# Kernel tuning notes

Hardware: AMD Instinct MI355X
Metric: run time of the kernel (lower is better)

## Reference

```python
import jax, jax.numpy as jnp
import numpy as np

B, L, D, H = 2, 2048, 1024, 16
DK = D // H


def setup_inputs() -> dict:
    key = jax.random.key(0)
    ks = jax.random.split(key, 12)
    s = 1.0 / np.sqrt(D)
    inp = {
        "query": jax.random.normal(ks[0], (B, L, D), jnp.float32),
        "key_": jax.random.normal(ks[1], (B, L, D), jnp.float32),
        "value": jax.random.normal(ks[2], (B, L, D), jnp.float32),
        # causal boolean mask, broadcast over heads: (B, 1, L_q, L_k)
        "mask": jnp.broadcast_to(jnp.tril(jnp.ones((L, L), jnp.bool_)), (B, 1, L, L)),
        "w_q": jax.random.uniform(ks[3], (D, D), jnp.float32, -s, s),
        "b_q": jax.random.uniform(ks[4], (D,), jnp.float32, -s, s),
        "w_k": jax.random.uniform(ks[5], (D, D), jnp.float32, -s, s),
        "b_k": jax.random.uniform(ks[6], (D,), jnp.float32, -s, s),
        "w_v": jax.random.uniform(ks[7], (D, D), jnp.float32, -s, s),
        "b_v": jax.random.uniform(ks[8], (D,), jnp.float32, -s, s),
        "w_o": jax.random.uniform(ks[9], (D, D), jnp.float32, -s, s),
        "b_o": jax.random.uniform(ks[10], (D,), jnp.float32, -s, s),
    }
    return inp


def reference(query, key_, value, mask, w_q, b_q, w_k, b_k, w_v, b_v, w_o, b_o):
    # torch nn.Linear: y = x @ W.T + b, weight shape (out, in)
    Q = query @ w_q.T + b_q
    K = key_ @ w_k.T + b_k
    V = value @ w_v.T + b_v
    # (B, L, H, DK) -> (B, H, L, DK)
    Q = Q.reshape(B, L, H, DK).transpose(0, 2, 1, 3)
    K = K.reshape(B, L, H, DK).transpose(0, 2, 1, 3)
    V = V.reshape(B, L, H, DK).transpose(0, 2, 1, 3)
    scaling = jnp.sqrt(jnp.float32(DK))
    scores = jnp.einsum("bhqd,bhkd->bhqk", Q, K) / scaling  # (B,H,L,L)
    scores = jnp.where(mask, scores, jnp.float32(-1e9))
    attn = jax.nn.softmax(scores, axis=-1)
    out = jnp.einsum("bhqk,bhkd->bhqd", attn, V)  # (B,H,L,DK)
    out = out.transpose(0, 2, 1, 3).reshape(B, L, D)
    return out @ w_o.T + b_o
```

## Files before the change

### kernel.cpp

```cpp
#include <hip/hip_runtime.h>
#include <stdint.h>

#define Bb 2
#define Ll 2048
#define Dd 1024
#define Hh 16
#define DKd 64
#define Mm (Bb*Ll)

typedef __bf16 bf16_t;
typedef __bf16 bf16x8 __attribute__((ext_vector_type(8)));
typedef float f32x4 __attribute__((ext_vector_type(4)));
typedef unsigned u32x2 __attribute__((ext_vector_type(2)));

#define AS1C(p) ((const __attribute__((address_space(1))) void*)(p))
#define AS3(p)  ((__attribute__((address_space(3))) void*)(p))

__device__ __forceinline__ unsigned short bfu(float f){
  return __builtin_bit_cast(unsigned short, (bf16_t)f);
}
__device__ __forceinline__ void wait_vm4(){ asm volatile("s_waitcnt vmcnt(4)" ::: "memory"); }
__device__ __forceinline__ void wait_vm6(){ asm volatile("s_waitcnt vmcnt(6)" ::: "memory"); }
__device__ __forceinline__ void wait_vm0(){ asm volatile("s_waitcnt vmcnt(0)" ::: "memory"); }
__device__ __forceinline__ void bar(){
  __builtin_amdgcn_sched_barrier(0);
  __builtin_amdgcn_s_barrier();
  __builtin_amdgcn_sched_barrier(0);
}

struct Cvt7 { const float* in[7]; ushort4* out[7]; int n4[7]; };

__global__ void cvt_multi(Cvt7 a){
  const int z = blockIdx.y;
  int i = blockIdx.x*256 + threadIdx.x;
  if (i < a.n4[z]){
    float4 v = ((const float4*)a.in[z])[i];
    ushort4 o; o.x=bfu(v.x); o.y=bfu(v.y); o.z=bfu(v.z); o.w=bfu(v.w);
    a.out[z][i] = o;
  }
}

#define BM 128
#define BN 64
#define BKs 64

struct GemmArgs {
  const bf16_t* A[3];
  const bf16_t* W[3];
  const float*  bias[3];
  void*         out[3];
  float         scale[3];
  int           mode[3];
};

__device__ __forceinline__ void stage_tile(
    const bf16_t* __restrict__ A, const bf16_t* __restrict__ Bw,
    int m0, int n0, int K, int k0, bf16_t* As, bf16_t* Bs,
    int w, int srow, int scol)
{
#pragma unroll
  for (int i = 0; i < 4; i++) {
    int c = i*4 + w;
    int row = c*8 + srow;
    int sc = scol ^ ((row & 7) << 3);
    __builtin_amdgcn_global_load_lds(AS1C(A + (size_t)(m0+row)*K + k0 + sc),
                                     AS3(As + c*512), 16, 0, 0);
  }
#pragma unroll
  for (int i = 0; i < 2; i++) {
    int c = i*4 + w;
    int row = c*8 + srow;
    int sc = scol ^ ((row & 7) << 3);
    __builtin_amdgcn_global_load_lds(AS1C(Bw + (size_t)(n0+row)*K + k0 + sc),
                                     AS3(Bs + c*512), 16, 0, 0);
  }
}

__global__ __launch_bounds__(256) void gemm_bt(GemmArgs ga, int M, int N, int K)
{
  const int z = blockIdx.z;
  const bf16_t* __restrict__ A  = ga.A[z];
  const bf16_t* __restrict__ Bw = ga.W[z];
  const float*  __restrict__ bias = ga.bias[z];
  void* __restrict__ out = ga.out[z];
  const float scale = ga.scale[z];
  const int mode = ga.mode[z];

  __shared__ bf16_t As[2][BM*BKs];
  __shared__ bf16_t Bs[2][BN*BKs];
  const int tid = threadIdx.x;
  const int lane = tid & 63;
  const int w = tid >> 6;
  const int m0 = blockIdx.x * BM;
  const int n0 = blockIdx.y * BN;
  const int wr = (w >> 1) * 64, wc = (w & 1) * 32;
  const int lrow16 = lane & 15;
  const int kgrp = lane >> 4;
  const int srow = lane >> 3;
  const int scol = (lane & 7) * 8;

  f32x4 acc[4][2] = {};

  stage_tile(A, Bw, m0, n0, K, 0, As[0], Bs[0], w, srow, scol);

  const int KT = K / BKs;
  int cur = 0;
  for (int kt = 0; kt < KT; ++kt) {
    if (kt + 1 < KT) {
      stage_tile(A, Bw, m0, n0, K, (kt+1)*BKs, As[cur^1], Bs[cur^1], w, srow, scol);
      wait_vm6();
    } else {
      wait_vm0();
    }
    bar();
#pragma unroll
    for (int ks = 0; ks < 2; ++ks) {
      const int kbyte = ks*64 + kgrp*16;
      bf16x8 af[4], bfr[2];
#pragma unroll
      for (int m = 0; m < 4; m++) {
        int row = wr + m*16 + lrow16;
        af[m] = *(const bf16x8*)((const char*)As[cur] + row*128 + (kbyte ^ ((row & 7) << 4)));
      }
#pragma unroll
      for (int n = 0; n < 2; n++) {
        int row = wc + n*16 + lrow16;
        bfr[n] = *(const bf16x8*)((const char*)Bs[cur] + row*128 + (kbyte ^ ((row & 7) << 4)));
      }
#pragma unroll
      for (int m = 0; m < 4; m++)
#pragma unroll
        for (int n = 0; n < 2; n++)
          acc[m][n] = __builtin_amdgcn_mfma_f32_16x16x32_bf16(af[m], bfr[n], acc[m][n], 0, 0, 0);
    }
    bar();
    cur ^= 1;
  }

#pragma unroll
  for (int m = 0; m < 4; m++)
#pragma unroll
    for (int n = 0; n < 2; n++) {
      const int row0 = m0 + wr + m*16 + kgrp*4;
      const int col  = n0 + wc + n*16 + lrow16;
      const float bcol = bias[col];
      if (mode == 2) {
        int b = row0 >> 11, l0 = row0 & 2047;
        int h = col >> 6, dk = col & 63;
        ushort4 u;
        u.x = bfu((acc[m][n][0] + bcol) * scale);
        u.y = bfu((acc[m][n][1] + bcol) * scale);
        u.z = bfu((acc[m][n][2] + bcol) * scale);
        u.w = bfu((acc[m][n][3] + bcol) * scale);
        *(ushort4*)((unsigned short*)out + ((size_t)((b<<4) + h)*DKd + dk)*Ll + l0) = u;
      } else {
#pragma unroll
        for (int i = 0; i < 4; i++) {
          int row = row0 + i;
          float v = (acc[m][n][i] + bcol) * scale;
          if (mode == 1) {
            ((float*)out)[(size_t)row*N + col] = v;
          } else {
            int b = row >> 11, l = row & 2047;
            int h = col >> 6, dk = col & 63;
            ((unsigned short*)out)[((size_t)((b<<4) + h)*Ll + l)*DKd + dk] = bfu(v);
          }
        }
      }
    }
}

#define KVB 64

__global__ __launch_bounds__(256) void attn_kernel(
    const bf16_t* __restrict__ Qh, const bf16_t* __restrict__ Kh,
    const bf16_t* __restrict__ VTg, unsigned short* __restrict__ Oa)
{
  const int id = blockIdx.x;
  const int x = id & 7;
  const int rest = id >> 3;
  const int hq = rest >> 4;
  const int j  = rest & 15;
  const int bh = x + 8*hq;
  const int sA = j;
  const int qtB = 31 - j;

  const int tid = threadIdx.x, lane = tid & 63, w = tid >> 6;
  const int r = lane & 15, g = lane >> 4;

  const bf16_t* Qp  = Qh  + (size_t)bh * Ll * DKd;
  const bf16_t* Kp  = Kh  + (size_t)bh * Ll * DKd;
  const bf16_t* VTp = VTg + (size_t)bh * Ll * DKd;

  __shared__ bf16_t Klds[2][64*64];
  __shared__ bf16_t Vlds[2][64*64];
  __shared__ bf16_t Plds[4][16*64];

  int q0 = j * 64;
  bf16x8 qf[2], qB[2];
#pragma unroll
  for (int ks = 0; ks < 2; ++ks) {
    qf[ks] = *(const bf16x8*)(Qp + (size_t)(q0 + w*16 + r)*DKd + ks*32 + g*8);
    qB[ks] = *(const bf16x8*)(Qp + (size_t)(qtB*64 + w*16 + r)*DKd + ks*32 + g*8);
  }

  bf16x8 ones;
#pragma unroll
  for (int jj = 0; jj < 8; ++jj) ones[jj] = (bf16_t)1.0f;

  f32x4 accO[4] = {};
  f32x4 accL = {};
  float mrow = -1e30f;

  const int krow_l = lane >> 3;
  const int kcol_l = ((lane & 7)*16) ^ (krow_l << 4);
  char* Pw = (char*)&Plds[w][0];
  const int rsw = (r & 7) << 4;
  const int b_ = bh >> 4, h_ = bh & 15;

  auto pre_tiles = [&](int kv, int buf){
#pragma unroll
    for (int i = 0; i < 2; ++i) {
      int c = i*4 + w;
      __builtin_amdgcn_global_load_lds(
        AS1C((const char*)Kp + (size_t)(kv*KVB + c*8 + krow_l)*128 + kcol_l),
        AS3((char*)&Klds[buf][0] + c*1024), 16, 0, 0);
      __builtin_amdgcn_global_load_lds(
        AS1C((const char*)VTp + (size_t)(c*8 + krow_l)*4096 + kv*128 + kcol_l),
        AS3((char*)&Vlds[buf][0] + c*1024), 16, 0, 0);
    }
  };

  pre_tiles(0, 0);

  int cur = 0;
  for (int s = 0; s < 33; ++s) {
    if (s < 32) {
      int kv2 = (s < sA) ? s + 1 : s - sA;
      pre_tiles(kv2, cur^1);
      wait_vm4();
    } else {
      wait_vm0();
    }
    bar();

    const int kv0 = ((s <= sA) ? s : s - sA - 1) * KVB;

    const char* Kbase = (const char*)&Klds[cur][0];
    f32x4 sv[4] = {};
    __builtin_amdgcn_s_setprio(1);
#pragma unroll
    for (int ks = 0; ks < 2; ++ks) {
      const int kbyte = ks*64 + g*16;
#pragma unroll
      for (int n = 0; n < 4; ++n) {
        int row = n*16 + r;
        bf16x8 kf = *(const bf16x8*)(Kbase + row*128 + (kbyte ^ ((row & 7) << 4)));
        sv[n] = __builtin_amdgcn_mfma_f32_16x16x32_bf16(kf, qf[ks], sv[n], 0, 0, 0);
      }
    }
    __builtin_amdgcn_s_setprio(0);

    if (s == sA || s == 32) {
      const int qg = q0 + w*16 + r;
#pragma unroll
      for (int n = 0; n < 4; ++n)
#pragma unroll
        for (int i = 0; i < 4; ++i)
          if (kv0 + n*16 + g*4 + i > qg) sv[n][i] = -1e30f;
    }

    float m0 = fmaxf(fmaxf(sv[0][0], sv[0][1]), sv[0][2]);
    float m1 = fmaxf(fmaxf(sv[0][3], sv[1][0]), sv[1][1]);
    float m2 = fmaxf(fmaxf(sv[1][2], sv[1][3]), sv[2][0]);
    float m3 = fmaxf(fmaxf(sv[2][1], sv[2][2]), sv[2][3]);
    float m4 = fmaxf(fmaxf(sv[3][0], sv[3][1]), sv[3][2]);
    float mx = fmaxf(fmaxf(fmaxf(m0, m1), m2), fmaxf(fmaxf(m3, m4), sv[3][3]));
    if (__any(mx > mrow + 8.f)) {
      mx = fmaxf(mx, __shfl_xor(mx, 16));
      mx = fmaxf(mx, __shfl_xor(mx, 32));
      float mnew = fmaxf(mrow, mx);
      float corr = __builtin_amdgcn_exp2f(mrow - mnew);
      float c0 = __shfl(corr, g*4 + 0);
      float c1 = __shfl(corr, g*4 + 1);
      float c2 = __shfl(corr, g*4 + 2);
      float c3 = __shfl(corr, g*4 + 3);
#pragma unroll
      for (int n = 0; n < 4; ++n) {
        accO[n][0] *= c0; accO[n][1] *= c1; accO[n][2] *= c2; accO[n][3] *= c3;
      }
      accL[0] *= c0; accL[1] *= c1; accL[2] *= c2; accL[3] *= c3;
      mrow = mnew;
    }
#pragma unroll
    for (int n = 0; n < 4; ++n)
#pragma unroll
      for (int i = 0; i < 4; ++i)
        sv[n][i] = __builtin_amdgcn_exp2f(sv[n][i] - mrow);

#pragma unroll
    for (int n = 0; n < 4; ++n) {
      unsigned lo = (unsigned)bfu(sv[n][0]) | ((unsigned)bfu(sv[n][1]) << 16);
      unsigned hi = (unsigned)bfu(sv[n][2]) | ((unsigned)bfu(sv[n][3]) << 16);
      u32x2 pk; pk[0] = lo; pk[1] = hi;
      *(u32x2*)(Pw + r*128 + ((n*32 + g*8) ^ rsw)) = pk;
    }

    const char* Vbase = (const char*)&Vlds[cur][0];
    __builtin_amdgcn_s_setprio(1);
#pragma unroll
    for (int ks = 0; ks < 2; ++ks) {
      const int kbyte = ks*64 + g*16;
      bf16x8 pa = *(const bf16x8*)(Pw + r*128 + (kbyte ^ rsw));
      accL = __builtin_amdgcn_mfma_f32_16x16x32_bf16(pa, ones, accL, 0, 0, 0);
#pragma unroll
      for (int n = 0; n < 4; ++n) {
        int row = n*16 + r;
        bf16x8 vf = *(const bf16x8*)(Vbase + row*128 + (kbyte ^ ((row & 7) << 4)));
        accO[n] = __builtin_amdgcn_mfma_f32_16x16x32_bf16(pa, vf, accO[n], 0, 0, 0);
      }
    }
    __builtin_amdgcn_s_setprio(0);

    if (s == sA) {
#pragma unroll
      for (int i = 0; i < 4; ++i) {
        float inv = 1.f / accL[i];
        int q = q0 + w*16 + g*4 + i;
#pragma unroll
        for (int n = 0; n < 4; ++n)
          Oa[((size_t)(b_*Ll + q))*Dd + h_*DKd + n*16 + r] = bfu(accO[n][i] * inv);
      }
      q0 = qtB * 64;
      qf[0] = qB[0]; qf[1] = qB[1];
#pragma unroll
      for (int n = 0; n < 4; ++n) accO[n] = f32x4{};
      accL = f32x4{};
      mrow = -1e30f;
    }

    bar();
    cur ^= 1;
  }

#pragma unroll
  for (int i = 0; i < 4; ++i) {
    float inv = 1.f / accL[i];
    int q = q0 + w*16 + g*4 + i;
#pragma unroll
    for (int n = 0; n < 4; ++n)
      Oa[((size_t)(b_*Ll + q))*Dd + h_*DKd + n*16 + r] = bfu(accO[n][i] * inv);
  }
}

extern "C" void kernel_launch(void* const* d_in, const int* in_sizes, int n_in,
                              void* d_out, int out_size, void* d_ws, size_t ws_size,
                              hipStream_t stream)
{
  const float* q  = (const float*)d_in[0];
  const float* k  = (const float*)d_in[1];
  const float* v  = (const float*)d_in[2];
  const float* wq = (const float*)d_in[4];
  const float* bq = (const float*)d_in[5];
  const float* wk = (const float*)d_in[6];
  const float* bk = (const float*)d_in[7];
  const float* wv = (const float*)d_in[8];
  const float* bv = (const float*)d_in[9];
  const float* wo = (const float*)d_in[10];
  const float* bo = (const float*)d_in[11];

  char* ws = (char*)d_ws;
  bf16_t* Xq = (bf16_t*)(ws + 0);
  bf16_t* Xk = (bf16_t*)(ws + 8388608);
  bf16_t* Xv = (bf16_t*)(ws + 16777216);
  bf16_t* Wq = (bf16_t*)(ws + 25165824);
  bf16_t* Wk = (bf16_t*)(ws + 27262976);
  bf16_t* Wv = (bf16_t*)(ws + 29360128);
  bf16_t* Wo = (bf16_t*)(ws + 31457280);
  bf16_t* Qh = (bf16_t*)(ws + 33554432);
  bf16_t* Kh = (bf16_t*)(ws + 41943040);
  bf16_t* VT = (bf16_t*)(ws + 50331648);
  bf16_t* Oa = (bf16_t*)(ws + 58720256);

  const int NX4 = Mm * Dd / 4;
  const int NW4 = Dd * Dd / 4;

  Cvt7 cv;
  cv.in[0]=q;  cv.out[0]=(ushort4*)Xq; cv.n4[0]=NX4;
  cv.in[1]=k;  cv.out[1]=(ushort4*)Xk; cv.n4[1]=NX4;
  cv.in[2]=v;  cv.out[2]=(ushort4*)Xv; cv.n4[2]=NX4;
  cv.in[3]=wq; cv.out[3]=(ushort4*)Wq; cv.n4[3]=NW4;
  cv.in[4]=wk; cv.out[4]=(ushort4*)Wk; cv.n4[4]=NW4;
  cv.in[5]=wv; cv.out[5]=(ushort4*)Wv; cv.n4[5]=NW4;
  cv.in[6]=wo; cv.out[6]=(ushort4*)Wo; cv.n4[6]=NW4;
  cvt_multi<<<dim3(NX4/256, 7), 256, 0, stream>>>(cv);

  const float qscale = 0.125f * 1.4426950408889634f;
  GemmArgs gqkv;
  gqkv.A[0]=Xq; gqkv.A[1]=Xk; gqkv.A[2]=Xv;
  gqkv.W[0]=Wq; gqkv.W[1]=Wk; gqkv.W[2]=Wv;
  gqkv.bias[0]=bq; gqkv.bias[1]=bk; gqkv.bias[2]=bv;
  gqkv.out[0]=Qh; gqkv.out[1]=Kh; gqkv.out[2]=VT;
  gqkv.scale[0]=qscale; gqkv.scale[1]=1.0f; gqkv.scale[2]=1.0f;
  gqkv.mode[0]=0; gqkv.mode[1]=0; gqkv.mode[2]=2;
  gemm_bt<<<dim3(Mm/BM, Dd/BN, 3), 256, 0, stream>>>(gqkv, Mm, Dd, Dd);

  attn_kernel<<<dim3(512), 256, 0, stream>>>(Qh, Kh, VT, (unsigned short*)Oa);

  GemmArgs go;
  go.A[0]=Oa; go.A[1]=Oa; go.A[2]=Oa;
  go.W[0]=Wo; go.W[1]=Wo; go.W[2]=Wo;
  go.bias[0]=bo; go.bias[1]=bo; go.bias[2]=bo;
  go.out[0]=d_out; go.out[1]=d_out; go.out[2]=d_out;
  go.scale[0]=1.0f; go.scale[1]=1.0f; go.scale[2]=1.0f;
  go.mode[0]=1; go.mode[1]=1; go.mode[2]=1;
  gemm_bt<<<dim3(Mm/BM, Dd/BN, 1), 256, 0, stream>>>(go, Mm, Dd, Dd);
}
```

Before: 117.3 us.

## Use a 128x128-tile GEMM kernel for the fused QKV projection

Adds a gemm128 kernel with 128x128 output tiles in which each wave computes a 64x64 sub-tile (4x4 MFMA 16x16x32 bf16 accumulators), and uses it for the batched Q/K/V projection in place of the 128x64 gemm_bt. Larger tiles raise arithmetic intensity and cut redundant A-tile loads across N-blocks. The new kernel is single-buffered, with a sync after each k-step and no prefetch overlap. It also uses more accumulator registers and launches half as many blocks (768), which may lower occupancy and latency hiding compared with the old pipelined kernel.

```diff
diff --git a/kernel.cpp b/kernel.cpp
--- a/kernel.cpp
+++ b/kernel.cpp
@@ -39,10 +39,6 @@
     a.out[z][i] = o;
   }
 }
-
-#define BM 128
-#define BN 64
-#define BKs 64
 
 struct GemmArgs {
   const bf16_t* A[3];
@@ -52,6 +48,110 @@
   float         scale[3];
   int           mode[3];
 };
+
+#define BKs 64
+
+__global__ __launch_bounds__(256) void gemm128(GemmArgs ga, int M, int N, int K)
+{
+  const int z = blockIdx.z;
+  const bf16_t* __restrict__ A  = ga.A[z];
+  const bf16_t* __restrict__ Bw = ga.W[z];
+  const float*  __restrict__ bias = ga.bias[z];
+  void* __restrict__ out = ga.out[z];
+  const float scale = ga.scale[z];
+  const int mode = ga.mode[z];
+
+  __shared__ bf16_t As[128*BKs];
+  __shared__ bf16_t Bs[128*BKs];
+  const int tid = threadIdx.x;
+  const int lane = tid & 63;
+  const int w = tid >> 6;
+  const int m0 = blockIdx.x * 128;
+  const int n0 = blockIdx.y * 128;
+  const int wr = (w >> 1) * 64, wc = (w & 1) * 64;
+  const int lrow16 = lane & 15;
+  const int kgrp = lane >> 4;
+  const int srow = lane >> 3;
+  const int scol = (lane & 7) * 8;
+
+  f32x4 acc[4][4] = {};
+
+  for (int k0 = 0; k0 < K; k0 += BKs) {
+#pragma unroll
+    for (int i = 0; i < 4; i++) {
+      int c = i*4 + w;
+      int row = c*8 + srow;
+      int sc = scol ^ ((row & 7) << 3);
+      __builtin_amdgcn_global_load_lds(AS1C(A + (size_t)(m0+row)*K + k0 + sc),
+                                       AS3(As + c*512), 16, 0, 0);
+    }
+#pragma unroll
+    for (int i = 0; i < 4; i++) {
+      int c = i*4 + w;
+      int row = c*8 + srow;
+      int sc = scol ^ ((row & 7) << 3);
+      __builtin_amdgcn_global_load_lds(AS1C(Bw + (size_t)(n0+row)*K + k0 + sc),
+                                       AS3(Bs + c*512), 16, 0, 0);
+    }
+    __syncthreads();
+#pragma unroll
+    for (int ks = 0; ks < 2; ++ks) {
+      const int kbyte = ks*64 + kgrp*16;
+      bf16x8 af[4], bfr[4];
+#pragma unroll
+      for (int m = 0; m < 4; m++) {
+        int row = wr + m*16 + lrow16;
+        af[m] = *(const bf16x8*)((const char*)As + row*128 + (kbyte ^ ((row & 7) << 4)));
+      }
+#pragma unroll
+      for (int n = 0; n < 4; n++) {
+        int row = wc + n*16 + lrow16;
+        bfr[n] = *(const bf16x8*)((const char*)Bs + row*128 + (kbyte ^ ((row & 7) << 4)));
+      }
+#pragma unroll
+      for (int m = 0; m < 4; m++)
+#pragma unroll
+        for (int n = 0; n < 4; n++)
+          acc[m][n] = __builtin_amdgcn_mfma_f32_16x16x32_bf16(af[m], bfr[n], acc[m][n], 0, 0, 0);
+    }
+    __syncthreads();
+  }
+
+#pragma unroll
+  for (int m = 0; m < 4; m++)
+#pragma unroll
+    for (int n = 0; n < 4; n++) {
+      const int row0 = m0 + wr + m*16 + kgrp*4;
+      const int col  = n0 + wc + n*16 + lrow16;
+      const float bcol = bias[col];
+      if (mode == 2) {
+        int b = row0 >> 11, l0 = row0 & 2047;
+        int h = col >> 6, dk = col & 63;
+        ushort4 u;
+        u.x = bfu((acc[m][n][0] + bcol) * scale);
+        u.y = bfu((acc[m][n][1] + bcol) * scale);
+        u.z = bfu((acc[m][n][2] + bcol) * scale);
+        u.w = bfu((acc[m][n][3] + bcol) * scale);
+        *(ushort4*)((unsigned short*)out + ((size_t)((b<<4) + h)*DKd + dk)*Ll + l0) = u;
+      } else {
+#pragma unroll
+        for (int i = 0; i < 4; i++) {
+          int row = row0 + i;
+          float v = (acc[m][n][i] + bcol) * scale;
+          if (mode == 1) {
+            ((float*)out)[(size_t)row*N + col] = v;
+          } else {
+            int b = row >> 11, l = row & 2047;
+            int h = col >> 6, dk = col & 63;
+            ((unsigned short*)out)[((size_t)((b<<4) + h)*Ll + l)*DKd + dk] = bfu(v);
+          }
+        }
+      }
+    }
+}
+
+#define BM 128
+#define BN 64
 
 __device__ __forceinline__ void stage_tile(
     const bf16_t* __restrict__ A, const bf16_t* __restrict__ Bw,
@@ -403,7 +503,7 @@
   gqkv.out[0]=Qh; gqkv.out[1]=Kh; gqkv.out[2]=VT;
   gqkv.scale[0]=qscale; gqkv.scale[1]=1.0f; gqkv.scale[2]=1.0f;
   gqkv.mode[0]=0; gqkv.mode[1]=0; gqkv.mode[2]=2;
-  gemm_bt<<<dim3(Mm/BM, Dd/BN, 3), 256, 0, stream>>>(gqkv, Mm, Dd, Dd);
+  gemm128<<<dim3(Mm/128, Dd/128, 3), 256, 0, stream>>>(gqkv, Mm, Dd, Dd);
 
   attn_kernel<<<dim3(512), 256, 0, stream>>>(Qh, Kh, VT, (unsigned short*)Oa);
 
```

Result: faster. 113.6 us (-3.1%).
